# Kernel optimization log

Hardware: AMD Instinct MI355X
Metric: run time of the kernel (lower is better)

## Reference

```python
import jax, jax.numpy as jnp
import numpy as np

EPS = 1e-9
ROUTINGS = 3
B, H, CIN, COUT = 16, 8, 32, 32


def setup_inputs() -> dict:
    key = jax.random.key(0)
    k1, k2 = jax.random.split(key)
    # activations/poses from a previous capsule layer are in [0,1) after squashing/sigmoid
    x = jax.random.uniform(k1, (B, H, H, CIN * 17), dtype=jnp.float32)
    w = jax.random.normal(k2, (1, CIN, COUT, 4, 4), dtype=jnp.float32)  # TruncatedNormal(std=1) ~ normal
    beta_v = jnp.zeros((COUT, 18), jnp.float32)
    beta_a = jnp.zeros((COUT,), jnp.float32)
    ij = jnp.stack(jnp.meshgrid(jnp.arange(H), jnp.arange(H), indexing='ij'), axis=-1)
    coord_add = ij.reshape(H * H, 2).astype(jnp.float32) / H  # [H*H, 2] scaled coords
    return {"x": x, "w": w, "beta_v": beta_v, "beta_a": beta_a, "coord_add": coord_add}


def em_routing(votes, activation, beta_v, beta_a, routings):
    # votes: [N, ci, co, ch=18], activation: [N, ci, 1]
    N, ci, co, ch = votes.shape
    r = jnp.full((N, ci, co), 1.0 / co, dtype=votes.dtype)
    miu = sigma_sq = act_out = None
    for it in range(routings):  # small fixed routing count
        if it > 0:
            # E-step: Gaussian log-likelihood of each vote under each output capsule
            log_p = -0.5 * jnp.log(sigma_sq) - jnp.square(votes - miu) / (2.0 * sigma_sq)  # [N,ci,co,ch]
            log_p = log_p - (jnp.max(log_p, axis=(2, 3), keepdims=True) - jnp.log(10.0))
            p = jnp.exp(jnp.sum(log_p, axis=3))  # [N,ci,co]
            ap = p * act_out.reshape(N, 1, co)
            r = ap / (jnp.sum(ap, axis=2, keepdims=True) + EPS)
        # M-step
        r = r * activation  # weight by input activation, broadcast over co
        r = r / (jnp.sum(r, axis=2, keepdims=True) + EPS)
        r_sum = jnp.sum(r, axis=1, keepdims=True)  # [N,1,co]
        r1 = (r / (r_sum + EPS))[..., None]        # [N,ci,co,1]
        miu = jnp.sum(votes * r1, axis=1, keepdims=True)                        # [N,1,co,ch]
        sigma_sq = jnp.sum(jnp.square(votes - miu) * r1, axis=1, keepdims=True) + EPS
        if it == routings - 1:
            rs = r_sum.reshape(N, co, 1)
            cost_h = (beta_v + 0.5 * jnp.log(sigma_sq.reshape(N, co, ch))) * rs  # [N,co,ch]
            ac_lambda = 0.01 * (it + 1)
            act_out = jax.nn.softmax(ac_lambda * (beta_a - jnp.sum(cost_h, axis=2)), axis=-1)
        else:
            act_out = jax.nn.softmax(r_sum.reshape(N, co), axis=-1)
    return miu, act_out


def reference(x, w, beta_v, beta_a, coord_add):
    Bx, Hx, Wx, C = x.shape
    ci = C // 17
    xr = x.reshape(Bx, Hx, Wx, ci, 17)
    pose = xr[..., :16].reshape(-1, ci, 16)   # [N, ci, 16], N = B*H*W
    act = xr[..., 16].reshape(-1, ci, 1)      # [N, ci, 1]
    N = pose.shape[0]
    co = w.shape[2]
    # mat_transform: batched 4x4 matmul pose @ w per (input capsule, output capsule)
    votes = jnp.einsum('niab,icbd->nicad', pose.reshape(N, ci, 4, 4), w[0]).reshape(N, ci, co, 16)
    # coordinate addition: 2 extra channels with spatial coords, tiled over batch/capsules
    coord = jnp.broadcast_to(coord_add.reshape(Hx * Wx, 1, 1, 2), (Hx * Wx, ci, co, 2))
    coord = jnp.tile(coord, (Bx, 1, 1, 1))    # [N, ci, co, 2]
    votes = jnp.concatenate([coord, votes], axis=3)  # [N, ci, co, 18]
    miu, act_out = em_routing(votes, act, beta_v, beta_a, ROUTINGS)
    # global average pool over the spatial grid
    outputs = jnp.mean(act_out.reshape(Bx, Hx, Wx, co), axis=(1, 2))                       # [B, co]
    pose_out = jnp.mean(miu.reshape(Bx, Hx, Wx, co * 18), axis=(1, 2)).reshape(Bx, co, 18)  # [B, co, 18]
    return outputs, pose_out
```

## Files before the change

### kernel.cpp

```cpp
#include <hip/hip_runtime.h>
#include <math.h>


#define CI 32
#define CO 32
#define CH 18
#define NPOS 1024
#define OUT_ACT (16 * 32)
#define OUT_TOTAL (OUT_ACT + 16 * CO * CH)

constexpr float EPSF = 1e-9f;
constexpr float LN10 = 2.302585092994046f;

__device__ __forceinline__ float fast_rcp(float x) {
    return __builtin_amdgcn_rcpf(x);
}

template <int CTRL>
__device__ __forceinline__ float dppf(float x) {
    union { float f; int i; } u; u.f = x;
    u.i = __builtin_amdgcn_update_dpp(u.i, u.i, CTRL, 0xF, 0xF, true);
    return u.f;
}

__device__ __forceinline__ float bf_sum32(float x) {
    x += dppf<0xB1>(x);
    x += dppf<0x4E>(x);
    x += dppf<0x141>(x);
    x += dppf<0x140>(x);
    x += __shfl_xor(x, 16);
    return x;
}
__device__ __forceinline__ float bf_max32(float x) {
    x = fmaxf(x, dppf<0xB1>(x));
    x = fmaxf(x, dppf<0x4E>(x));
    x = fmaxf(x, dppf<0x141>(x));
    x = fmaxf(x, dppf<0x140>(x));
    x = fmaxf(x, __shfl_xor(x, 16));
    return x;
}

__global__ __launch_bounds__(256, 4) void caps_em_kernel(
    const float* __restrict__ x,
    const float* __restrict__ w,
    const float* __restrict__ beta_v,
    const float* __restrict__ beta_a,
    const float* __restrict__ coord_add,
    float* __restrict__ out)
{
    const int n  = blockIdx.x;
    const int t  = threadIdx.x;
    const int c  = t & 31;
    const int ig = t >> 5;
    const int wv = t >> 6;

    __shared__ float  pose[CI][16];
    __shared__ float  act_in[CI];
    __shared__ float  rs_part[4][CO];
    __shared__ float2 part2[4][CO * 19];
    __shared__ float2 muq_s[CO * 19];
    __shared__ float  base_s[CO * 19];

    const float* xrow = x + n * (CI * 17);
    for (int e = t; e < CI * 17; e += 256) {
        int i = e / 17, k = e % 17;
        float val = xrow[e];
        if (k < 16) pose[i][k] = val;
        else        act_in[i]  = val;
    }
    const float cx = coord_add[(n & 63) * 2 + 0];
    const float cy = coord_add[(n & 63) * 2 + 1];
    __syncthreads();

    float v[4][16];
    #pragma unroll
    for (int k = 0; k < 4; ++k) {
        int i = ig * 4 + k;
        float wr[16];
        const float4* wp4 = (const float4*)(w + ((i * CO + c) << 4));
        #pragma unroll
        for (int q = 0; q < 4; ++q) {
            float4 wf = wp4[q];
            wr[q*4+0] = wf.x; wr[q*4+1] = wf.y; wr[q*4+2] = wf.z; wr[q*4+3] = wf.w;
        }
        float pr[16];
        const float4* pp4 = (const float4*)pose[i];
        #pragma unroll
        for (int q = 0; q < 4; ++q) {
            float4 pf = pp4[q];
            pr[q*4+0] = pf.x; pr[q*4+1] = pf.y; pr[q*4+2] = pf.z; pr[q*4+3] = pf.w;
        }
        #pragma unroll
        for (int a = 0; a < 4; ++a) {
            #pragma unroll
            for (int d = 0; d < 4; ++d) {
                float s = pr[a*4+0] * wr[0*4+d];
                s += pr[a*4+1] * wr[1*4+d];
                s += pr[a*4+2] * wr[2*4+d];
                s += pr[a*4+3] * wr[3*4+d];
                v[k][a*4+d] = s;
            }
        }
    }

    float rr[4];
    float act_c = 0.0f;
    float r_sum;

    for (int it = 0; it < 3; ++it) {
        if (it > 0) {
            float S[4], mx[4];
            #pragma unroll
            for (int k = 0; k < 4; ++k) { S[k] = 0.0f; mx[k] = -3.0e38f; }
            #pragma unroll
            for (int ch = 0; ch < CH; ++ch) {
                float2 mq = muq_s[c * 19 + ch];
                float  bs = base_s[c * 19 + ch];
                #pragma unroll
                for (int k = 0; k < 4; ++k) {
                    float vv = (ch == 0) ? cx
                             : ((ch == 1) ? cy : v[k][ch - 2]);
                    float d  = vv - mq.x;
                    float lp = bs - d * d * mq.y;
                    S[k] += lp;
                    mx[k] = fmaxf(mx[k], lp);
                }
            }
            #pragma unroll
            for (int k = 0; k < 4; ++k) {
                float m = bf_max32(mx[k]);
                float shift = 18.0f * (m - LN10);
                float pe = __expf(S[k] - shift);
                float ap = pe * act_c;
                float A  = bf_sum32(ap);
                float invA = fast_rcp(A + EPSF);
                float re = ap * invA;
                float sk = A * invA;
                float an = act_in[ig * 4 + k];
                rr[k] = re * an * fast_rcp(an * sk + EPSF);
            }
        } else {
            #pragma unroll
            for (int k = 0; k < 4; ++k) {
                float an = act_in[ig * 4 + k];
                rr[k] = (1.0f / 32.0f) * an * fast_rcp(an + EPSF);
            }
        }

        {
            float prr = rr[0] + rr[1] + rr[2] + rr[3];
            float prs = prr + __shfl_xor(prr, 32);
            rs_part[wv][c] = prs;
            float2* pp = &part2[wv][c * 19];
            float s0 = cx * prr, s1 = cy * prr;
            s0 += __shfl_xor(s0, 32);
            s1 += __shfl_xor(s1, 32);
            pp[0] = make_float2(s0, cx * s0);
            pp[1] = make_float2(s1, cy * s1);
            #pragma unroll
            for (int ch = 2; ch < CH; ++ch) {
                float s = 0.0f, s2 = 0.0f;
                #pragma unroll
                for (int k = 0; k < 4; ++k) {
                    float rv = rr[k] * v[k][ch - 2];
                    s  += rv;
                    s2 += rv * v[k][ch - 2];
                }
                s  += __shfl_xor(s, 32);
                s2 += __shfl_xor(s2, 32);
                pp[ch] = make_float2(s, s2);
            }
        }
        __syncthreads();

        {
            float rs = rs_part[0][c] + rs_part[1][c]
                     + rs_part[2][c] + rs_part[3][c];
            r_sum = rs;
            float rsinv = fast_rcp(rs + EPSF);
            float s1 = rs * rsinv;
            float c2 = 2.0f - s1;
            for (int ch = ig; ch < CH; ch += 8) {
                int j = c * 19 + ch;
                float2 a0 = part2[0][j], a1 = part2[1][j];
                float2 a2 = part2[2][j], a3 = part2[3][j];
                float mu_un = a0.x + a1.x + a2.x + a3.x;
                float v2_un = a0.y + a1.y + a2.y + a3.y;
                float mu  = mu_un * rsinv;
                float sig = fmaxf(v2_un * rsinv - mu * mu * c2, 0.0f) + EPSF;
                muq_s[j]  = make_float2(mu, 0.5f * fast_rcp(sig));
                base_s[j] = -0.5f * __logf(sig);
            }
        }
        __syncthreads();

        {
            float logit;
            if (it == 2) {
                float cost = 0.0f;
                #pragma unroll
                for (int ch = 0; ch < CH; ++ch)
                    cost += beta_v[c * CH + ch] - base_s[c * 19 + ch];
                logit = 0.03f * (beta_a[c] - cost * r_sum);
            } else {
                logit = r_sum;
            }
            float mxl = bf_max32(logit);
            float ex  = __expf(logit - mxl);
            act_c = ex * fast_rcp(bf_sum32(ex));
        }
    }

    const float inv64 = 1.0f / 64.0f;
    const int b = n >> 6;
    if (t < CO)
        atomicAdd(&out[b * CO + t], act_c * inv64);
    for (int e = t; e < CO * CH; e += 256) {
        int cc = e / CH, ch = e - cc * CH;
        atomicAdd(&out[OUT_ACT + b * (CO * CH) + e], muq_s[cc * 19 + ch].x * inv64);
    }
}

extern "C" void kernel_launch(void* const* d_in, const int* in_sizes, int n_in,
                              void* d_out, int out_size, void* d_ws, size_t ws_size,
                              hipStream_t stream) {
    const float* x         = (const float*)d_in[0];
    const float* w         = (const float*)d_in[1];
    const float* beta_v    = (const float*)d_in[2];
    const float* beta_a    = (const float*)d_in[3];
    const float* coord_add = (const float*)d_in[4];
    float* out = (float*)d_out;

    hipMemsetAsync(out, 0, (size_t)OUT_TOTAL * sizeof(float), stream);
    caps_em_kernel<<<dim3(NPOS), dim3(256), 0, stream>>>(
        x, w, beta_v, beta_a, coord_add, out);
}
```

Baseline: 84.21 us.

## Replace global atomic pooling with per-position workspace writes plus reduction kernel

Each block now writes its 608 per-position outputs (activations and means) to a workspace instead of atomically adding into the pooled output. A second small kernel sums the 64 spatial positions per batch element and writes the final averages, which also drops the memset. This removes contention from 1024 blocks doing atomics onto 16 output rows, at the cost of an extra kernel launch, a workspace round trip, and a reduction kernel with only 16 blocks. The old atomic path is kept as a fallback when no workspace is available.

```diff
diff --git a/kernel.cpp b/kernel.cpp
--- a/kernel.cpp
+++ b/kernel.cpp
@@ -8,6 +8,7 @@
 #define NPOS 1024
 #define OUT_ACT (16 * 32)
 #define OUT_TOTAL (OUT_ACT + 16 * CO * CH)
+#define PPOS 608
 
 constexpr float EPSF = 1e-9f;
 constexpr float LN10 = 2.302585092994046f;
@@ -40,13 +41,14 @@
     return x;
 }
 
+template <int MODE>
 __global__ __launch_bounds__(256, 4) void caps_em_kernel(
     const float* __restrict__ x,
     const float* __restrict__ w,
     const float* __restrict__ beta_v,
     const float* __restrict__ beta_a,
     const float* __restrict__ coord_add,
-    float* __restrict__ out)
+    float* __restrict__ dst)
 {
     const int n  = blockIdx.x;
     const int t  = threadIdx.x;
@@ -211,13 +213,41 @@
         }
     }
 
+    if (MODE == 0) {
+        float* sp = dst + (size_t)n * PPOS;
+        if (t < CO) sp[t] = act_c;
+        for (int e = t; e < CO * CH; e += 256) {
+            int cc = e / CH, ch = e - cc * CH;
+            sp[CO + e] = muq_s[cc * 19 + ch].x;
+        }
+    } else {
+        const float inv64 = 1.0f / 64.0f;
+        const int b = n >> 6;
+        if (t < CO)
+            atomicAdd(&dst[b * CO + t], act_c * inv64);
+        for (int e = t; e < CO * CH; e += 256) {
+            int cc = e / CH, ch = e - cc * CH;
+            atomicAdd(&dst[OUT_ACT + b * (CO * CH) + e],
+                      muq_s[cc * 19 + ch].x * inv64);
+        }
+    }
+}
+
+__global__ __launch_bounds__(256) void caps_reduce_kernel(
+    const float* __restrict__ ws, float* __restrict__ out)
+{
+    const int b = blockIdx.x;
+    const int t = threadIdx.x;
     const float inv64 = 1.0f / 64.0f;
-    const int b = n >> 6;
-    if (t < CO)
-        atomicAdd(&out[b * CO + t], act_c * inv64);
-    for (int e = t; e < CO * CH; e += 256) {
-        int cc = e / CH, ch = e - cc * CH;
-        atomicAdd(&out[OUT_ACT + b * (CO * CH) + e], muq_s[cc * 19 + ch].x * inv64);
+    const float* sb = ws + (size_t)(b * 64) * PPOS;
+    for (int j = t; j < PPOS; j += 256) {
+        float s = 0.0f;
+        #pragma unroll 4
+        for (int p = 0; p < 64; ++p)
+            s += sb[p * PPOS + j];
+        s *= inv64;
+        if (j < CO) out[b * CO + j] = s;
+        else        out[OUT_ACT + b * (CO * CH) + (j - CO)] = s;
     }
 }
 
@@ -230,8 +260,16 @@
     const float* beta_a    = (const float*)d_in[3];
     const float* coord_add = (const float*)d_in[4];
     float* out = (float*)d_out;
-
-    hipMemsetAsync(out, 0, (size_t)OUT_TOTAL * sizeof(float), stream);
-    caps_em_kernel<<<dim3(NPOS), dim3(256), 0, stream>>>(
-        x, w, beta_v, beta_a, coord_add, out);
-}
+    float* ws  = (float*)d_ws;
+
+    const size_t need = (size_t)NPOS * PPOS * sizeof(float);
+    if (ws != nullptr && ws_size >= need) {
+        caps_em_kernel<0><<<dim3(NPOS), dim3(256), 0, stream>>>(
+            x, w, beta_v, beta_a, coord_add, ws);
+        caps_reduce_kernel<<<dim3(16), dim3(256), 0, stream>>>(ws, out);
+    } else {
+        hipMemsetAsync(out, 0, (size_t)OUT_TOTAL * sizeof(float), stream);
+        caps_em_kernel<1><<<dim3(NPOS), dim3(256), 0, stream>>>(
+            x, w, beta_v, beta_a, coord_add, out);
+    }
+}
```

Measured after the change: 97.87 us. 16.2% more time.
